# Optimization experiments

Measured on AMD Instinct MI355X. Metric: run time of the kernel, lower is better.

The kernel has to match this reference:

```python
import jax, jax.numpy as jnp
import numpy as np

EMBED_DIM = 1024
NUM_HEADS = 16
HEAD_DIM = EMBED_DIM // NUM_HEADS
SCALING = HEAD_DIM ** -0.5


def setup_inputs() -> dict:
    key = jax.random.key(0)
    ks = jax.random.split(key, 11)
    B, S, E = 4, 2048, EMBED_DIM
    s = 1.0 / np.sqrt(E)
    return {
        "query": jax.random.normal(ks[0], (B, S, E), jnp.float32),
        "key": jax.random.normal(ks[1], (B, S, E), jnp.float32),
        "value": jax.random.normal(ks[2], (B, S, E), jnp.float32),
        "q_w": jax.random.normal(ks[3], (E, E), jnp.float32) * s,
        "q_b": jax.random.normal(ks[4], (E,), jnp.float32) * 0.01,
        "k_w": jax.random.normal(ks[5], (E, E), jnp.float32) * s,
        "k_b": jax.random.normal(ks[6], (E,), jnp.float32) * 0.01,
        "v_w": jax.random.normal(ks[7], (E, E), jnp.float32) * s,
        "v_b": jax.random.normal(ks[8], (E,), jnp.float32) * 0.01,
        "out_w": jax.random.normal(ks[9], (E, E), jnp.float32) * s,
        "out_b": jax.random.normal(ks[10], (E,), jnp.float32) * 0.01,
    }


def reference(query, key, value, q_w, q_b, k_w, k_b, v_w, v_b, out_w, out_b):
    B, S, E = query.shape
    H, D = NUM_HEADS, HEAD_DIM
    # torch Linear: x @ W.T + b
    q = (query @ q_w.T + q_b).reshape(B, S, H, D).transpose(0, 2, 1, 3)  # [B,H,S,D]
    k = (key @ k_w.T + k_b).reshape(B, -1, H, D).transpose(0, 2, 1, 3)
    v = (value @ v_w.T + v_b).reshape(B, -1, H, D).transpose(0, 2, 1, 3)
    attn_scores = jnp.einsum("bhsd,bhtd->bhst", q, k) * SCALING  # [B,H,S,S]
    attn_weights = jax.nn.softmax(attn_scores, axis=-1)
    attn_output = jnp.einsum("bhst,bhtd->bhsd", attn_weights, v)
    attn_output = attn_output.transpose(0, 2, 1, 3).reshape(B, S, E)
    return attn_output @ out_w.T + out_b
```

## Files before the change

### kernel.cpp

```cpp
#include <hip/hip_runtime.h>
#include <stdint.h>
#include <stddef.h>

#define BB 4
#define SS 2048
#define EE 1024
#define HH 16
#define DD 64
#define MTOT (BB * SS)

#define SOFTMAX_C (0.125f * 1.44269504088896340736f)

using bf16x8 = __attribute__((ext_vector_type(8))) __bf16;
using f32x4  = __attribute__((ext_vector_type(4))) float;

__device__ inline unsigned short f2bf(float f) {
    union { float f; uint32_t u; } v; v.f = f;
    uint32_t u = v.u;
    u += 0x7fffu + ((u >> 16) & 1u);
    return (unsigned short)(u >> 16);
}

__global__ __launch_bounds__(256) void cast_f32_bf16(
    const float* __restrict__ in, unsigned short* __restrict__ out, int n4) {
    int i = blockIdx.x * 256 + threadIdx.x;
    if (i < n4) {
        float4 f = ((const float4*)in)[i];
        ushort4 o;
        o.x = f2bf(f.x); o.y = f2bf(f.y); o.z = f2bf(f.z); o.w = f2bf(f.w);
        ((ushort4*)out)[i] = o;
    }
}

template <int MODE>
__global__ __launch_bounds__(256) void gemm_nt(
    const unsigned short* __restrict__ A,
    const unsigned short* __restrict__ W,
    const float* __restrict__ bias,
    void* __restrict__ outp) {
    constexpr int LS = 72;
    __shared__ __align__(16) unsigned short As[128 * LS];
    __shared__ __align__(16) unsigned short Bs[128 * LS];

    const int tid  = threadIdx.x;
    const int lane = tid & 63;
    const int wid  = tid >> 6;
    const int wm   = wid >> 1;
    const int wn   = wid & 1;
    const int quad = lane >> 4;
    const int l16  = lane & 15;
    const int m0   = blockIdx.y * 128;
    const int n0   = blockIdx.x * 128;

    f32x4 acc[4][4];
#pragma unroll
    for (int i = 0; i < 4; i++)
#pragma unroll
        for (int j = 0; j < 4; j++) acc[i][j] = (f32x4){0.f, 0.f, 0.f, 0.f};

    for (int k0 = 0; k0 < 1024; k0 += 64) {
        __syncthreads();
#pragma unroll
        for (int i = 0; i < 4; i++) {
            int c = tid + 256 * i;
            int row = c >> 3;
            int col8 = (c & 7) * 8;
            uint4 av = *(const uint4*)(A + (size_t)(m0 + row) * 1024 + k0 + col8);
            *(uint4*)(As + row * LS + col8) = av;
            uint4 bv = *(const uint4*)(W + (size_t)(n0 + row) * 1024 + k0 + col8);
            *(uint4*)(Bs + row * LS + col8) = bv;
        }
        __syncthreads();

#pragma unroll
        for (int kt = 0; kt < 2; kt++) {
            bf16x8 a[4], b[4];
#pragma unroll
            for (int mt = 0; mt < 4; mt++)
                a[mt] = *(const bf16x8*)(As + (wm * 64 + mt * 16 + l16) * LS + kt * 32 + quad * 8);
#pragma unroll
            for (int nt = 0; nt < 4; nt++)
                b[nt] = *(const bf16x8*)(Bs + (wn * 64 + nt * 16 + l16) * LS + kt * 32 + quad * 8);
#pragma unroll
            for (int mt = 0; mt < 4; mt++)
#pragma unroll
                for (int nt = 0; nt < 4; nt++)
                    acc[mt][nt] = __builtin_amdgcn_mfma_f32_16x16x32_bf16(
                        a[mt], b[nt], acc[mt][nt], 0, 0, 0);
        }
    }

#pragma unroll
    for (int mt = 0; mt < 4; mt++) {
#pragma unroll
        for (int nt = 0; nt < 4; nt++) {
            int gcol = n0 + wn * 64 + nt * 16 + l16;
            float bv = bias[gcol];
#pragma unroll
            for (int r = 0; r < 4; r++) {
                int grow = m0 + wm * 64 + mt * 16 + quad * 4 + r;
                float v = acc[mt][nt][r] + bv;
                if (MODE == 0) {
                    int bb = grow >> 11, sr = grow & 2047;
                    int hh = gcol >> 6,  dd = gcol & 63;
                    ((unsigned short*)outp)[(((size_t)(bb * HH + hh)) * SS + sr) * DD + dd] = f2bf(v);
                } else if (MODE == 2) {
                    int bb = grow >> 11, sr = grow & 2047;
                    int hh = gcol >> 6,  dd = gcol & 63;
                    ((unsigned short*)outp)[(((size_t)(bb * HH + hh)) * DD + dd) * SS + sr] = f2bf(v);
                } else {
                    ((float*)outp)[(size_t)grow * 1024 + gcol] = v;
                }
            }
        }
    }
}

__global__ __launch_bounds__(256) void flash_attn2(
    const unsigned short* __restrict__ Qh,
    const unsigned short* __restrict__ Kh,
    const unsigned short* __restrict__ Vtg,
    unsigned short* __restrict__ attn) {
    constexpr int LS = 72;
    __shared__ __align__(16) unsigned short Sh[128 * LS];
    unsigned short* Ks = Sh;
    unsigned short* Vs = Sh + 64 * LS;

    const int tid  = threadIdx.x;
    const int lane = tid & 63;
    const int w    = tid >> 6;
    const int quad = lane >> 4;
    const int l16  = lane & 15;
    const int bh   = blockIdx.y;
    const int q0   = blockIdx.x * 128;
    const size_t base = (size_t)bh * SS * DD;

    bf16x8 bq[2][2];
#pragma unroll
    for (int s = 0; s < 2; s++)
#pragma unroll
        for (int kt = 0; kt < 2; kt++)
            bq[s][kt] = *(const bf16x8*)(Qh + base +
                (size_t)(q0 + w * 32 + s * 16 + l16) * DD + kt * 32 + quad * 8);

    float l_part[2] = {0.f, 0.f};
    f32x4 oT[2][4];
#pragma unroll
    for (int s = 0; s < 2; s++)
#pragma unroll
        for (int dt = 0; dt < 4; dt++) oT[s][dt] = (f32x4){0.f, 0.f, 0.f, 0.f};

    const int srcLaneA = ((2 * (quad & 1)) * 16 + l16) << 2;
    const int srcLaneB = ((2 * (quad & 1) + 1) * 16 + l16) << 2;

    for (int j0 = 0; j0 < SS; j0 += 64) {
        __syncthreads();
#pragma unroll
        for (int i = 0; i < 2; i++) {
            int c = tid + 256 * i;
            int row = c >> 3, col8 = (c & 7) * 8;
            *(uint4*)(Ks + row * LS + col8) =
                *(const uint4*)(Kh + base + (size_t)(j0 + row) * DD + col8);
            *(uint4*)(Vs + row * LS + col8) =
                *(const uint4*)(Vtg + base + (size_t)row * SS + j0 + col8);
        }
        __syncthreads();

        f32x4 sacc[2][4];
#pragma unroll
        for (int s = 0; s < 2; s++)
#pragma unroll
            for (int mt = 0; mt < 4; mt++) sacc[s][mt] = (f32x4){0.f, 0.f, 0.f, 0.f};
#pragma unroll
        for (int kt = 0; kt < 2; kt++) {
            bf16x8 ak[4];
#pragma unroll
            for (int mt = 0; mt < 4; mt++)
                ak[mt] = *(const bf16x8*)(Ks + (mt * 16 + l16) * LS + kt * 32 + quad * 8);
#pragma unroll
            for (int s = 0; s < 2; s++)
#pragma unroll
                for (int mt = 0; mt < 4; mt++)
                    sacc[s][mt] = __builtin_amdgcn_mfma_f32_16x16x32_bf16(
                        ak[mt], bq[s][kt], sacc[s][mt], 0, 0, 0);
        }

        uint32_t ppk[2][4][2];
#pragma unroll
        for (int s = 0; s < 2; s++) {
#pragma unroll
            for (int mt = 0; mt < 4; mt++) {
                float p0 = __builtin_amdgcn_exp2f(sacc[s][mt][0] * SOFTMAX_C);
                float p1 = __builtin_amdgcn_exp2f(sacc[s][mt][1] * SOFTMAX_C);
                float p2 = __builtin_amdgcn_exp2f(sacc[s][mt][2] * SOFTMAX_C);
                float p3 = __builtin_amdgcn_exp2f(sacc[s][mt][3] * SOFTMAX_C);
                l_part[s] += (p0 + p1) + (p2 + p3);
                ppk[s][mt][0] = (uint32_t)f2bf(p0) | ((uint32_t)f2bf(p1) << 16);
                ppk[s][mt][1] = (uint32_t)f2bf(p2) | ((uint32_t)f2bf(p3) << 16);
            }
        }

#pragma unroll
        for (int kt = 0; kt < 2; kt++) {
            bf16x8 av[4];
#pragma unroll
            for (int dt = 0; dt < 4; dt++)
                av[dt] = *(const bf16x8*)(Vs + (dt * 16 + l16) * LS + kt * 32 + quad * 8);
#pragma unroll
            for (int s = 0; s < 2; s++) {
                union { uint32_t wds[4]; bf16x8 v; } bp;
#pragma unroll
                for (int jp = 0; jp < 4; jp++) {
                    int sl = (jp < 2) ? srcLaneA : srcLaneB;
                    uint32_t lo = (uint32_t)__builtin_amdgcn_ds_bpermute(
                        sl, (int)ppk[s][2 * kt][jp & 1]);
                    uint32_t hi = (uint32_t)__builtin_amdgcn_ds_bpermute(
                        sl, (int)ppk[s][2 * kt + 1][jp & 1]);
                    bp.wds[jp] = (quad < 2) ? lo : hi;
                }
#pragma unroll
                for (int dt = 0; dt < 4; dt++)
                    oT[s][dt] = __builtin_amdgcn_mfma_f32_16x16x32_bf16(
                        av[dt], bp.v, oT[s][dt], 0, 0, 0);
            }
        }
    }

    float inv_l[2];
#pragma unroll
    for (int s = 0; s < 2; s++) {
        float l = l_part[s];
        l += __shfl_xor(l, 16, 64);
        l += __shfl_xor(l, 32, 64);
        inv_l[s] = 1.f / l;
    }

    __syncthreads();
#pragma unroll
    for (int s = 0; s < 2; s++)
#pragma unroll
        for (int dt = 0; dt < 4; dt++)
#pragma unroll
            for (int r = 0; r < 4; r++)
                Sh[(w * 32 + s * 16 + l16) * LS + dt * 16 + quad * 4 + r] =
                    f2bf(oT[s][dt][r] * inv_l[s]);
    __syncthreads();

    const int b = bh >> 4, h = bh & 15;
#pragma unroll
    for (int i = 0; i < 4; i++) {
        int c = tid + 256 * i;
        int row = c >> 3, col8 = (c & 7) * 8;
        *(uint4*)(attn + ((size_t)b * SS + q0 + row) * EE + h * 64 + col8) =
            *(const uint4*)(Sh + row * LS + col8);
    }
}

extern "C" void kernel_launch(void* const* d_in, const int* in_sizes, int n_in,
                              void* d_out, int out_size, void* d_ws, size_t ws_size,
                              hipStream_t stream) {
    (void)in_sizes; (void)n_in; (void)out_size; (void)ws_size;
    const float* q_in  = (const float*)d_in[0];
    const float* k_in  = (const float*)d_in[1];
    const float* v_in  = (const float*)d_in[2];
    const float* q_w   = (const float*)d_in[3];
    const float* q_b   = (const float*)d_in[4];
    const float* k_w   = (const float*)d_in[5];
    const float* k_b   = (const float*)d_in[6];
    const float* v_w   = (const float*)d_in[7];
    const float* v_b   = (const float*)d_in[8];
    const float* out_w = (const float*)d_in[9];
    const float* out_b = (const float*)d_in[10];

    const size_t NX = (size_t)MTOT * EE;
    const size_t NW = (size_t)EE * EE;

    unsigned short* xq = (unsigned short*)d_ws;
    unsigned short* xk = xq + NX;
    unsigned short* xv = xk + NX;
    unsigned short* wq = xv + NX;
    unsigned short* wk = wq + NW;
    unsigned short* wv = wk + NW;
    unsigned short* wo = wv + NW;
    unsigned short* qh = wo + NW;
    unsigned short* kh = qh + NX;
    unsigned short* vt = kh + NX;
    unsigned short* attn = vt + NX;

    cast_f32_bf16<<<(int)(NX / 4 / 256), 256, 0, stream>>>(q_in, xq, (int)(NX / 4));
    cast_f32_bf16<<<(int)(NX / 4 / 256), 256, 0, stream>>>(k_in, xk, (int)(NX / 4));
    cast_f32_bf16<<<(int)(NX / 4 / 256), 256, 0, stream>>>(v_in, xv, (int)(NX / 4));
    cast_f32_bf16<<<(int)(NW / 4 / 256), 256, 0, stream>>>(q_w, wq, (int)(NW / 4));
    cast_f32_bf16<<<(int)(NW / 4 / 256), 256, 0, stream>>>(k_w, wk, (int)(NW / 4));
    cast_f32_bf16<<<(int)(NW / 4 / 256), 256, 0, stream>>>(v_w, wv, (int)(NW / 4));
    cast_f32_bf16<<<(int)(NW / 4 / 256), 256, 0, stream>>>(out_w, wo, (int)(NW / 4));

    dim3 ggrid(EE / 128, MTOT / 128);
    gemm_nt<0><<<ggrid, 256, 0, stream>>>(xq, wq, q_b, qh);
    gemm_nt<0><<<ggrid, 256, 0, stream>>>(xk, wk, k_b, kh);
    gemm_nt<2><<<ggrid, 256, 0, stream>>>(xv, wv, v_b, vt);

    flash_attn2<<<dim3(SS / 128, BB * HH), 256, 0, stream>>>(qh, kh, vt, attn);

    gemm_nt<1><<<ggrid, 256, 0, stream>>>(attn, wo, out_b, (float*)d_out);
}
```

Measured before the change: 415.8 us.

## Batch cast launches, use direct global-to-LDS GEMM loads, fold softmax scale, drop attention LDS staging

Replaces the seven separate cast launches with two batched launches that use blockIdx.y to pick the tensor. The GEMM now fills LDS with global_load_lds (16-byte direct loads) into an unpadded 64-wide tile, removing the register round-trip. The softmax scale is folded into the Q projection epilogue, so the attention kernel no longer multiplies each score before exp2. The attention kernel also reads K and V fragments straight from global memory instead of staging them through LDS with two barriers per tile. In exchange, the unpadded LDS rows may cause bank conflicts on the MFMA fragment reads, and the four waves now fetch the same K/V data redundantly through the cache.

```diff
diff --git a/kernel.cpp b/kernel.cpp
--- a/kernel.cpp
+++ b/kernel.cpp
@@ -21,14 +21,44 @@
     return (unsigned short)(u >> 16);
 }
 
-__global__ __launch_bounds__(256) void cast_f32_bf16(
-    const float* __restrict__ in, unsigned short* __restrict__ out, int n4) {
+__device__ inline void gld_lds16(const unsigned short* g, unsigned short* l) {
+    __builtin_amdgcn_global_load_lds(
+        (const __attribute__((address_space(1))) unsigned int*)g,
+        (__attribute__((address_space(3))) unsigned int*)l,
+        16, 0, 0);
+}
+
+__global__ __launch_bounds__(256) void cast3_f32_bf16(
+    const float* __restrict__ a, const float* __restrict__ b,
+    const float* __restrict__ c,
+    unsigned short* __restrict__ oa, unsigned short* __restrict__ ob,
+    unsigned short* __restrict__ oc, int n4) {
     int i = blockIdx.x * 256 + threadIdx.x;
+    const float* src = (blockIdx.y == 0) ? a : (blockIdx.y == 1) ? b : c;
+    unsigned short* dst = (blockIdx.y == 0) ? oa : (blockIdx.y == 1) ? ob : oc;
     if (i < n4) {
-        float4 f = ((const float4*)in)[i];
+        float4 f = ((const float4*)src)[i];
         ushort4 o;
         o.x = f2bf(f.x); o.y = f2bf(f.y); o.z = f2bf(f.z); o.w = f2bf(f.w);
-        ((ushort4*)out)[i] = o;
+        ((ushort4*)dst)[i] = o;
+    }
+}
+
+__global__ __launch_bounds__(256) void cast4_f32_bf16(
+    const float* __restrict__ a, const float* __restrict__ b,
+    const float* __restrict__ c, const float* __restrict__ d,
+    unsigned short* __restrict__ oa, unsigned short* __restrict__ ob,
+    unsigned short* __restrict__ oc, unsigned short* __restrict__ od, int n4) {
+    int i = blockIdx.x * 256 + threadIdx.x;
+    const float* src = (blockIdx.y == 0) ? a : (blockIdx.y == 1) ? b
+                     : (blockIdx.y == 2) ? c : d;
+    unsigned short* dst = (blockIdx.y == 0) ? oa : (blockIdx.y == 1) ? ob
+                        : (blockIdx.y == 2) ? oc : od;
+    if (i < n4) {
+        float4 f = ((const float4*)src)[i];
+        ushort4 o;
+        o.x = f2bf(f.x); o.y = f2bf(f.y); o.z = f2bf(f.z); o.w = f2bf(f.w);
+        ((ushort4*)dst)[i] = o;
     }
 }
 
@@ -37,11 +67,9 @@
     const unsigned short* __restrict__ A,
     const unsigned short* __restrict__ W,
     const float* __restrict__ bias,
-    void* __restrict__ outp) {
-    constexpr int LS = 72;
-    __shared__ __align__(16) unsigned short As[128 * LS];
-    __shared__ __align__(16) unsigned short Bs[128 * LS];
-
+    void* __restrict__ outp, float oscale) {
+    __shared__ __align__(16) unsigned short As[128 * 64];
+    __shared__ __align__(16) unsigned short Bs[128 * 64];
     const int tid  = threadIdx.x;
     const int lane = tid & 63;
     const int wid  = tid >> 6;
@@ -58,17 +86,19 @@
 #pragma unroll
         for (int j = 0; j < 4; j++) acc[i][j] = (f32x4){0.f, 0.f, 0.f, 0.f};
 
+    const int lrow = lane >> 3;
+    const int lcol = (lane & 7) * 8;
+    const unsigned short* ga = A + (size_t)(m0 + wid * 32 + lrow) * 1024 + lcol;
+    const unsigned short* gb = W + (size_t)(n0 + wid * 32 + lrow) * 1024 + lcol;
+    unsigned short* la = As + wid * 32 * 64;
+    unsigned short* lb = Bs + wid * 32 * 64;
+
     for (int k0 = 0; k0 < 1024; k0 += 64) {
         __syncthreads();
 #pragma unroll
-        for (int i = 0; i < 4; i++) {
-            int c = tid + 256 * i;
-            int row = c >> 3;
-            int col8 = (c & 7) * 8;
-            uint4 av = *(const uint4*)(A + (size_t)(m0 + row) * 1024 + k0 + col8);
-            *(uint4*)(As + row * LS + col8) = av;
-            uint4 bv = *(const uint4*)(W + (size_t)(n0 + row) * 1024 + k0 + col8);
-            *(uint4*)(Bs + row * LS + col8) = bv;
+        for (int c = 0; c < 4; c++) {
+            gld_lds16(ga + (size_t)c * 8 * 1024 + k0, la + c * 8 * 64);
+            gld_lds16(gb + (size_t)c * 8 * 1024 + k0, lb + c * 8 * 64);
         }
         __syncthreads();
 
@@ -77,10 +107,10 @@
             bf16x8 a[4], b[4];
 #pragma unroll
             for (int mt = 0; mt < 4; mt++)
-                a[mt] = *(const bf16x8*)(As + (wm * 64 + mt * 16 + l16) * LS + kt * 32 + quad * 8);
+                a[mt] = *(const bf16x8*)(As + (wm * 64 + mt * 16 + l16) * 64 + kt * 32 + quad * 8);
 #pragma unroll
             for (int nt = 0; nt < 4; nt++)
-                b[nt] = *(const bf16x8*)(Bs + (wn * 64 + nt * 16 + l16) * LS + kt * 32 + quad * 8);
+                b[nt] = *(const bf16x8*)(Bs + (wn * 64 + nt * 16 + l16) * 64 + kt * 32 + quad * 8);
 #pragma unroll
             for (int mt = 0; mt < 4; mt++)
 #pragma unroll
@@ -99,7 +129,7 @@
 #pragma unroll
             for (int r = 0; r < 4; r++) {
                 int grow = m0 + wm * 64 + mt * 16 + quad * 4 + r;
-                float v = acc[mt][nt][r] + bv;
+                float v = (acc[mt][nt][r] + bv) * oscale;
                 if (MODE == 0) {
                     int bb = grow >> 11, sr = grow & 2047;
                     int hh = gcol >> 6,  dd = gcol & 63;
@@ -116,15 +146,13 @@
     }
 }
 
-__global__ __launch_bounds__(256) void flash_attn2(
+__global__ __launch_bounds__(256) void flash_attn3(
     const unsigned short* __restrict__ Qh,
     const unsigned short* __restrict__ Kh,
     const unsigned short* __restrict__ Vtg,
     unsigned short* __restrict__ attn) {
     constexpr int LS = 72;
     __shared__ __align__(16) unsigned short Sh[128 * LS];
-    unsigned short* Ks = Sh;
-    unsigned short* Vs = Sh + 64 * LS;
 
     const int tid  = threadIdx.x;
     const int lane = tid & 63;
@@ -153,19 +181,10 @@
     const int srcLaneA = ((2 * (quad & 1)) * 16 + l16) << 2;
     const int srcLaneB = ((2 * (quad & 1) + 1) * 16 + l16) << 2;
 
+    const unsigned short* kp = Kh  + base + (size_t)l16 * DD + quad * 8;
+    const unsigned short* vp = Vtg + base + (size_t)l16 * SS + quad * 8;
+
     for (int j0 = 0; j0 < SS; j0 += 64) {
-        __syncthreads();
-#pragma unroll
-        for (int i = 0; i < 2; i++) {
-            int c = tid + 256 * i;
-            int row = c >> 3, col8 = (c & 7) * 8;
-            *(uint4*)(Ks + row * LS + col8) =
-                *(const uint4*)(Kh + base + (size_t)(j0 + row) * DD + col8);
-            *(uint4*)(Vs + row * LS + col8) =
-                *(const uint4*)(Vtg + base + (size_t)row * SS + j0 + col8);
-        }
-        __syncthreads();
-
         f32x4 sacc[2][4];
 #pragma unroll
         for (int s = 0; s < 2; s++)
@@ -176,7 +195,7 @@
             bf16x8 ak[4];
 #pragma unroll
             for (int mt = 0; mt < 4; mt++)
-                ak[mt] = *(const bf16x8*)(Ks + (mt * 16 + l16) * LS + kt * 32 + quad * 8);
+                ak[mt] = *(const bf16x8*)(kp + (size_t)(j0 + mt * 16) * DD + kt * 32);
 #pragma unroll
             for (int s = 0; s < 2; s++)
 #pragma unroll
@@ -190,10 +209,10 @@
         for (int s = 0; s < 2; s++) {
 #pragma unroll
             for (int mt = 0; mt < 4; mt++) {
-                float p0 = __builtin_amdgcn_exp2f(sacc[s][mt][0] * SOFTMAX_C);
-                float p1 = __builtin_amdgcn_exp2f(sacc[s][mt][1] * SOFTMAX_C);
-                float p2 = __builtin_amdgcn_exp2f(sacc[s][mt][2] * SOFTMAX_C);
-                float p3 = __builtin_amdgcn_exp2f(sacc[s][mt][3] * SOFTMAX_C);
+                float p0 = __builtin_amdgcn_exp2f(sacc[s][mt][0]);
+                float p1 = __builtin_amdgcn_exp2f(sacc[s][mt][1]);
+                float p2 = __builtin_amdgcn_exp2f(sacc[s][mt][2]);
+                float p3 = __builtin_amdgcn_exp2f(sacc[s][mt][3]);
                 l_part[s] += (p0 + p1) + (p2 + p3);
                 ppk[s][mt][0] = (uint32_t)f2bf(p0) | ((uint32_t)f2bf(p1) << 16);
                 ppk[s][mt][1] = (uint32_t)f2bf(p2) | ((uint32_t)f2bf(p3) << 16);
@@ -205,7 +224,7 @@
             bf16x8 av[4];
 #pragma unroll
             for (int dt = 0; dt < 4; dt++)
-                av[dt] = *(const bf16x8*)(Vs + (dt * 16 + l16) * LS + kt * 32 + quad * 8);
+                av[dt] = *(const bf16x8*)(vp + (size_t)(dt * 16) * SS + j0 + kt * 32);
 #pragma unroll
             for (int s = 0; s < 2; s++) {
                 union { uint32_t wds[4]; bf16x8 v; } bp;
@@ -235,7 +254,6 @@
         inv_l[s] = 1.f / l;
     }
 
-    __syncthreads();
 #pragma unroll
     for (int s = 0; s < 2; s++)
 #pragma unroll
@@ -287,20 +305,17 @@
     unsigned short* vt = kh + NX;
     unsigned short* attn = vt + NX;
 
-    cast_f32_bf16<<<(int)(NX / 4 / 256), 256, 0, stream>>>(q_in, xq, (int)(NX / 4));
-    cast_f32_bf16<<<(int)(NX / 4 / 256), 256, 0, stream>>>(k_in, xk, (int)(NX / 4));
-    cast_f32_bf16<<<(int)(NX / 4 / 256), 256, 0, stream>>>(v_in, xv, (int)(NX / 4));
-    cast_f32_bf16<<<(int)(NW / 4 / 256), 256, 0, stream>>>(q_w, wq, (int)(NW / 4));
-    cast_f32_bf16<<<(int)(NW / 4 / 256), 256, 0, stream>>>(k_w, wk, (int)(NW / 4));
-    cast_f32_bf16<<<(int)(NW / 4 / 256), 256, 0, stream>>>(v_w, wv, (int)(NW / 4));
-    cast_f32_bf16<<<(int)(NW / 4 / 256), 256, 0, stream>>>(out_w, wo, (int)(NW / 4));
+    cast3_f32_bf16<<<dim3((int)(NX / 4 / 256), 3), 256, 0, stream>>>(
+        q_in, k_in, v_in, xq, xk, xv, (int)(NX / 4));
+    cast4_f32_bf16<<<dim3((int)(NW / 4 / 256), 4), 256, 0, stream>>>(
+        q_w, k_w, v_w, out_w, wq, wk, wv, wo, (int)(NW / 4));
 
     dim3 ggrid(EE / 128, MTOT / 128);
-    gemm_nt<0><<<ggrid, 256, 0, stream>>>(xq, wq, q_b, qh);
-    gemm_nt<0><<<ggrid, 256, 0, stream>>>(xk, wk, k_b, kh);
-    gemm_nt<2><<<ggrid, 256, 0, stream>>>(xv, wv, v_b, vt);
-
-    flash_attn2<<<dim3(SS / 128, BB * HH), 256, 0, stream>>>(qh, kh, vt, attn);
-
-    gemm_nt<1><<<ggrid, 256, 0, stream>>>(attn, wo, out_b, (float*)d_out);
-}
+    gemm_nt<0><<<ggrid, 256, 0, stream>>>(xq, wq, q_b, qh, SOFTMAX_C);
+    gemm_nt<0><<<ggrid, 256, 0, stream>>>(xk, wk, k_b, kh, 1.0f);
+    gemm_nt<2><<<ggrid, 256, 0, stream>>>(xv, wv, v_b, vt, 1.0f);
+
+    flash_attn3<<<dim3(SS / 128, BB * HH), 256, 0, stream>>>(qh, kh, vt, attn);
+
+    gemm_nt<1><<<ggrid, 256, 0, stream>>>(attn, wo, out_b, (float*)d_out, 1.0f);
+}
```

Result: slower. 554.8 us (+33.4%).
